# Kernel optimization log

Hardware: AMD Instinct MI355X
Metric: run time of the kernel (lower is better)

The kernel has to match this reference:

```python
import jax, jax.numpy as jnp
import numpy as np

D_MODEL = 1024
NUM_HEADS = 16
D_HEAD = D_MODEL // NUM_HEADS


def _rope(x):
    """Rotary embedding, lucidrains interleaved convention, applied along axis -2.

    x: (..., n, d). Positions are arange(n); freq_i = 10000**(-2i/d), each freq
    repeated twice (interleaved); rotate_half swaps adjacent pairs (-x2, x1).
    """
    n, d = x.shape[-2], x.shape[-1]
    inv_freq = 1.0 / (10000.0 ** (jnp.arange(0, d, 2, dtype=jnp.float32) / d))  # (d/2,)
    freqs = jnp.arange(n, dtype=jnp.float32)[:, None] * inv_freq[None, :]       # (n, d/2)
    emb = jnp.repeat(freqs, 2, axis=-1)                                         # (n, d)
    cos, sin = jnp.cos(emb).astype(x.dtype), jnp.sin(emb).astype(x.dtype)
    xp = x.reshape(x.shape[:-1] + (d // 2, 2))
    rot = jnp.stack([-xp[..., 1], xp[..., 0]], axis=-1).reshape(x.shape)
    return x * cos + rot * sin


def setup_inputs() -> dict:
    key = jax.random.key(0)
    ks = jax.random.split(key, 11)
    B, S = 4, 2048
    mk = lambda k, shape: (jax.random.normal(k, shape, dtype=jnp.float32) * 0.02)
    return {
        "query": jax.random.normal(ks[0], (B, S, D_MODEL), dtype=jnp.float32),
        "key": jax.random.normal(ks[1], (B, S, D_MODEL), dtype=jnp.float32),
        "value": jax.random.normal(ks[2], (B, S, D_MODEL), dtype=jnp.float32),
        "Wq": mk(ks[3], (D_MODEL, D_MODEL)), "bq": jnp.zeros((D_MODEL,), jnp.float32),
        "Wk": mk(ks[4], (D_MODEL, D_MODEL)), "bk": jnp.zeros((D_MODEL,), jnp.float32),
        "Wv": mk(ks[5], (D_MODEL, D_MODEL)), "bv": jnp.zeros((D_MODEL,), jnp.float32),
        "Wo": mk(ks[6], (D_MODEL, D_MODEL)), "bo": jnp.zeros((D_MODEL,), jnp.float32),
    }


def reference(query, key, value, Wq, bq, Wk, bk, Wv, bv, Wo, bo):
    B, S, _ = query.shape
    H, dh = NUM_HEADS, D_HEAD
    # projections (torch Linear: x @ W.T + b)
    q = (query @ Wq.T + bq).reshape(B, S, H, dh)           # (b, t, h, d)
    k = (key @ Wk.T + bk).reshape(B, S, H, dh).transpose(0, 2, 1, 3)   # (b, h, t, d)
    v = (value @ Wv.T + bv).reshape(B, S, H, dh).transpose(0, 2, 1, 3)  # (b, h, t, d)
    # Faithful to source: query rotated along axis -2 = HEADS axis (pre-permute),
    # key rotated along axis -2 = time axis.
    q = _rope(q)                                            # positions over heads (source quirk)
    k = _rope(k)                                            # positions over time
    q = q.transpose(0, 2, 1, 3)                             # (b, h, t, d)
    scores = jnp.einsum("bhqd,bhkd->bhqk", q, k) / jnp.sqrt(jnp.float32(D_MODEL))
    attn = jax.nn.softmax(scores, axis=-1)
    ctx = jnp.einsum("bhqk,bhkd->bhqd", attn, v)            # (b, h, t, d)
    ctx = ctx.transpose(0, 2, 1, 3).reshape(B, S, H * dh)   # (b, t, d_model)
    return ctx @ Wo.T + bo
```

## Files before the change

kernel.cpp:

```cpp
#include <hip/hip_runtime.h>

using u16 = unsigned short;
typedef __bf16 bf16x8 __attribute__((ext_vector_type(8)));
typedef __bf16 bf16x2 __attribute__((ext_vector_type(2)));
typedef float f32x4 __attribute__((ext_vector_type(4)));

#if __has_builtin(__builtin_amdgcn_exp2f)
#define QSCALE 0.04508422468443852f
#define FEXP(x) __builtin_amdgcn_exp2f(x)
#else
#define QSCALE 0.03125f
#define FEXP(x) __expf(x)
#endif

__device__ __forceinline__ u16 f2bf(float f) {
  unsigned u = __builtin_bit_cast(unsigned, f);
  u += 0x7FFFu + ((u >> 16) & 1u);
  return (u16)(u >> 16);
}

#define GLD_LDS16(g, l)                                                                   \
  __builtin_amdgcn_global_load_lds((const __attribute__((address_space(1))) void*)(g),    \
                                   (__attribute__((address_space(3))) void*)(l), 16, 0, 0)

__global__ void cvt_all(const float* __restrict__ q, const float* __restrict__ k,
                        const float* __restrict__ v, const float* __restrict__ wq,
                        const float* __restrict__ wk, const float* __restrict__ wv,
                        const float* __restrict__ wo, u16* __restrict__ oq,
                        u16* __restrict__ ok, u16* __restrict__ ov, u16* __restrict__ owq,
                        u16* __restrict__ owk, u16* __restrict__ owv, u16* __restrict__ owo) {
  const float* in;
  u16* out;
  int n4, base, nb;
  const int bidx = blockIdx.x;
  if (bidx < 1536) {
    const int which = bidx >> 9;
    in = which == 0 ? q : which == 1 ? k : v;
    out = which == 0 ? oq : which == 1 ? ok : ov;
    n4 = 2097152; base = bidx & 511; nb = 512;
  } else {
    const int which = (bidx - 1536) >> 6;
    in = which == 0 ? wq : which == 1 ? wk : which == 2 ? wv : wo;
    out = which == 0 ? owq : which == 1 ? owk : which == 2 ? owv : owo;
    n4 = 262144; base = (bidx - 1536) & 63; nb = 64;
  }
  int i = base * blockDim.x + threadIdx.x;
  const int st = nb * blockDim.x;
  for (; i < n4; i += st) {
    float4 x = reinterpret_cast<const float4*>(in)[i];
    ushort4 o = make_ushort4(f2bf(x.x), f2bf(x.y), f2bf(x.z), f2bf(x.w));
    reinterpret_cast<ushort4*>(out)[i] = o;
  }
}

template <int EPI>
__global__ __launch_bounds__(512, 4) void gemm_bt(const u16* __restrict__ A,
                                                  const u16* __restrict__ Bt,
                                                  const float* __restrict__ bias,
                                                  void* __restrict__ outp) {
  __shared__ u16 lA[2][128 * 64];
  __shared__ u16 lB[2][128 * 64];
  const int tid = threadIdx.x;
  const int l = tid & 63, w = tid >> 6;
  const int wr = w >> 2, wc = w & 3;
  const int l15 = l & 15, lg = l >> 4;
  const int bid = ((blockIdx.x & 7) << 6) | (blockIdx.x >> 3);
  const int br = bid >> 3, bc = bid & 7;

  f32x4 acc[4][2];
#pragma unroll
  for (int m = 0; m < 4; ++m)
#pragma unroll
    for (int n = 0; n < 2; ++n) acc[m][n] = f32x4{0.f, 0.f, 0.f, 0.f};

  const int srow = tid >> 3;
  const int gch = (tid & 7) ^ (srow & 7);
  const u16* Abase = A + (size_t)(br * 128 + srow) * 1024 + gch * 8;
  const u16* Bbase = Bt + (size_t)(bc * 128 + srow) * 1024 + gch * 8;

  auto stage = [&](int buf, int kk) {
    GLD_LDS16(Abase + kk, &lA[buf][tid * 8]);
    GLD_LDS16(Abase + (size_t)64 * 1024 + kk, &lA[buf][4096 + tid * 8]);
    GLD_LDS16(Bbase + kk, &lB[buf][tid * 8]);
    GLD_LDS16(Bbase + (size_t)64 * 1024 + kk, &lB[buf][4096 + tid * 8]);
  };

  auto compute = [&](int cur) {
#pragma unroll
    for (int ks = 0; ks < 2; ++ks) {
      const int c = (((ks * 4 + lg) ^ (l15 & 7)) << 3);
      bf16x8 af[4], bfr[2];
#pragma unroll
      for (int m = 0; m < 4; ++m)
        af[m] = *reinterpret_cast<const bf16x8*>(&lA[cur][(wr * 64 + m * 16 + l15) * 64 + c]);
#pragma unroll
      for (int n = 0; n < 2; ++n)
        bfr[n] = *reinterpret_cast<const bf16x8*>(&lB[cur][(wc * 32 + n * 16 + l15) * 64 + c]);
#pragma unroll
      for (int m = 0; m < 4; ++m)
#pragma unroll
        for (int n = 0; n < 2; ++n)
          acc[m][n] = __builtin_amdgcn_mfma_f32_16x16x32_bf16(af[m], bfr[n], acc[m][n], 0, 0, 0);
    }
  };

  stage(0, 0);
  asm volatile("s_waitcnt vmcnt(0)" ::: "memory");
  __builtin_amdgcn_s_barrier();
  __builtin_amdgcn_sched_barrier(0);

  for (int it = 0; it < 16; ++it) {
    const int cur = it & 1;
    if (it < 15) stage(cur ^ 1, (it + 1) * 64);
    compute(cur);
    if (it < 15) {
      asm volatile("s_waitcnt vmcnt(0)" ::: "memory");
      __builtin_amdgcn_s_barrier();
      __builtin_amdgcn_sched_barrier(0);
    }
  }

  const int row0 = br * 128 + wr * 64;
  const int col0 = bc * 128 + wc * 32;

  if constexpr (EPI == 0 || EPI == 1) {
    u16* out = reinterpret_cast<u16*>(outp);
#pragma unroll
    for (int n = 0; n < 2; ++n) {
      const int gn = col0 + n * 16 + l15;
      const float bv2 = bias[gn];
      const int p = (gn & 63) >> 1;
      const float invf = __expf((float)p * -0.28782313663f);
      float ss = 0.f, cc = 0.f;
      if constexpr (EPI == 0) {
        const float th = (float)(gn >> 6) * invf;
        sincosf(th, &ss, &cc);
      }
#pragma unroll
      for (int m = 0; m < 4; ++m) {
        const int gm0 = row0 + m * 16 + lg * 4;
#pragma unroll
        for (int r = 0; r < 4; ++r) {
          float x = acc[m][n][r] + bv2;
          if constexpr (EPI == 1) {
            const float th = (float)((gm0 + r) & 2047) * invf;
            sincosf(th, &ss, &cc);
          }
          const float xp = __shfl_xor(x, 1);
          float o = (gn & 1) ? fmaf(xp, ss, x * cc) : fmaf(-xp, ss, x * cc);
          if constexpr (EPI == 0) o *= QSCALE;
          out[(size_t)(gm0 + r) * 1024 + gn] = f2bf(o);
        }
      }
    }
  } else if constexpr (EPI == 2) {
    u16* vT = reinterpret_cast<u16*>(outp);
#pragma unroll
    for (int n = 0; n < 2; ++n) {
      const int gn = col0 + n * 16 + l15;
      const float bv2 = bias[gn];
      const int hh = gn >> 6, dd = gn & 63;
#pragma unroll
      for (int m = 0; m < 4; ++m) {
        const int gm0 = row0 + m * 16 + lg * 4;
        const int bb = gm0 >> 11, s0 = gm0 & 2047;
        ushort4 pk = make_ushort4(f2bf(acc[m][n][0] + bv2), f2bf(acc[m][n][1] + bv2),
                                  f2bf(acc[m][n][2] + bv2), f2bf(acc[m][n][3] + bv2));
        *reinterpret_cast<ushort4*>(vT + ((size_t)((bb * 16 + hh) * 64 + dd) * 2048 + s0)) = pk;
      }
    }
  } else {
    float* out = reinterpret_cast<float*>(outp);
#pragma unroll
    for (int n = 0; n < 2; ++n) {
      const int gn = col0 + n * 16 + l15;
      const float bv2 = bias[gn];
#pragma unroll
      for (int m = 0; m < 4; ++m) {
        const int gm0 = row0 + m * 16 + lg * 4;
#pragma unroll
        for (int r = 0; r < 4; ++r) out[(size_t)(gm0 + r) * 1024 + gn] = acc[m][n][r] + bv2;
      }
    }
  }
}

__global__ __launch_bounds__(512, 4) void attn_fwd(const u16* __restrict__ Q,
                                                   const u16* __restrict__ K,
                                                   const u16* __restrict__ Vt,
                                                   u16* __restrict__ ctx) {
  __shared__ u16 sK[3][64 * 64];
  __shared__ u16 sV[3][64 * 64];
  const int tid = threadIdx.x;
  const int l = tid & 63, w = tid >> 6;
  const int l15 = l & 15, lg = l >> 4;
  const int swz = (l15 & 7) << 3;
  const int wgid = ((blockIdx.x & 7) << 6) | (blockIdx.x >> 3);
  const int qt = wgid & 7, bh = wgid >> 3;
  const int b = bh >> 4, h = bh & 15;

  bf16x8 qf[2][2];
#pragma unroll
  for (int g = 0; g < 2; ++g) {
    const u16* qp =
        Q + (size_t)(b * 2048 + qt * 256 + w * 32 + g * 16 + l15) * 1024 + h * 64 + lg * 8;
    qf[g][0] = *reinterpret_cast<const bf16x8*>(qp);
    qf[g][1] = *reinterpret_cast<const bf16x8*>(qp + 32);
  }

  bf16x8 ones;
#pragma unroll
  for (int i = 0; i < 8; ++i) ones[i] = (__bf16)1.0f;

  f32x4 acc_l[2];
  f32x4 acc_o[2][4];
#pragma unroll
  for (int g = 0; g < 2; ++g) {
    acc_l[g] = f32x4{0.f, 0.f, 0.f, 0.f};
#pragma unroll
    for (int n = 0; n < 4; ++n) acc_o[g][n] = f32x4{0.f, 0.f, 0.f, 0.f};
  }

  const int srow = tid >> 3;
  const int scol = ((tid & 7) ^ (srow & 7)) * 8;
  const int krow = (srow & 0x23) | ((srow & 0x0C) << 1) | ((srow & 0x10) >> 2);
  const u16* Kbase = K + (size_t)(b * 2048 + krow) * 1024 + h * 64 + scol;
  const u16* Vbase = Vt + (size_t)(bh * 64 + srow) * 2048 + scol;

  auto stage = [&](int buf, int j) {
    GLD_LDS16(Kbase + (size_t)(j * 64) * 1024, &sK[buf][tid * 8]);
    GLD_LDS16(Vbase + j * 64, &sV[buf][tid * 8]);
  };

  stage(0, 0);
  stage(1, 1);
  asm volatile("s_waitcnt vmcnt(2)" ::: "memory");
  __builtin_amdgcn_s_barrier();
  __builtin_amdgcn_sched_barrier(0);

  int cur = 0, nx2 = 2;
  for (int j = 0; j < 32; ++j) {
    if (j < 30) stage(nx2, j + 2);

    const int c0 = (lg * 8) ^ swz;
    f32x4 accs0[4], accs1[4];
#pragma unroll
    for (int nk = 0; nk < 4; ++nk) {
      accs0[nk] = f32x4{0.f, 0.f, 0.f, 0.f};
      accs1[nk] = f32x4{0.f, 0.f, 0.f, 0.f};
    }

    __builtin_amdgcn_s_setprio(1);
#pragma unroll
    for (int nk = 0; nk < 4; ++nk) {
      bf16x8 kf0 = *reinterpret_cast<const bf16x8*>(&sK[cur][(nk * 16 + l15) * 64 + c0]);
      bf16x8 kf1 = *reinterpret_cast<const bf16x8*>(&sK[cur][(nk * 16 + l15) * 64 + (c0 ^ 32)]);
      accs0[nk] = __builtin_amdgcn_mfma_f32_16x16x32_bf16(kf0, qf[0][0], accs0[nk], 0, 0, 0);
      accs0[nk] = __builtin_amdgcn_mfma_f32_16x16x32_bf16(kf1, qf[0][1], accs0[nk], 0, 0, 0);
      accs1[nk] = __builtin_amdgcn_mfma_f32_16x16x32_bf16(kf0, qf[1][0], accs1[nk], 0, 0, 0);
      accs1[nk] = __builtin_amdgcn_mfma_f32_16x16x32_bf16(kf1, qf[1][1], accs1[nk], 0, 0, 0);
    }
    __builtin_amdgcn_s_setprio(0);

    unsigned wpk0[4][2], wpk1[4][2];
#pragma unroll
    for (int nk = 0; nk < 4; ++nk) {
      const float p0 = FEXP(accs0[nk][0]), p1 = FEXP(accs0[nk][1]);
      const float p2 = FEXP(accs0[nk][2]), p3 = FEXP(accs0[nk][3]);
      bf16x2 t0, t1;
      t0.x = (__bf16)p0; t0.y = (__bf16)p1;
      t1.x = (__bf16)p2; t1.y = (__bf16)p3;
      wpk0[nk][0] = __builtin_bit_cast(unsigned, t0);
      wpk0[nk][1] = __builtin_bit_cast(unsigned, t1);
    }

    __builtin_amdgcn_s_setprio(1);
#pragma unroll
    for (int ks = 0; ks < 2; ++ks) {
      const uint4 paw = make_uint4(wpk0[2 * ks][0], wpk0[2 * ks][1],
                                   wpk0[2 * ks + 1][0], wpk0[2 * ks + 1][1]);
      const bf16x8 pa = __builtin_bit_cast(bf16x8, paw);
      acc_l[0] = __builtin_amdgcn_mfma_f32_16x16x32_bf16(ones, pa, acc_l[0], 0, 0, 0);
#pragma unroll
      for (int n = 0; n < 4; ++n) {
        bf16x8 vf = *reinterpret_cast<const bf16x8*>(
            &sV[cur][(n * 16 + l15) * 64 + ((ks * 32 + lg * 8) ^ swz)]);
        acc_o[0][n] = __builtin_amdgcn_mfma_f32_16x16x32_bf16(vf, pa, acc_o[0][n], 0, 0, 0);
      }
    }
    __builtin_amdgcn_s_setprio(0);

#pragma unroll
    for (int nk = 0; nk < 4; ++nk) {
      const float p0 = FEXP(accs1[nk][0]), p1 = FEXP(accs1[nk][1]);
      const float p2 = FEXP(accs1[nk][2]), p3 = FEXP(accs1[nk][3]);
      bf16x2 t0, t1;
      t0.x = (__bf16)p0; t0.y = (__bf16)p1;
      t1.x = (__bf16)p2; t1.y = (__bf16)p3;
      wpk1[nk][0] = __builtin_bit_cast(unsigned, t0);
      wpk1[nk][1] = __builtin_bit_cast(unsigned, t1);
    }

    __builtin_amdgcn_s_setprio(1);
#pragma unroll
    for (int ks = 0; ks < 2; ++ks) {
      const uint4 paw = make_uint4(wpk1[2 * ks][0], wpk1[2 * ks][1],
                                   wpk1[2 * ks + 1][0], wpk1[2 * ks + 1][1]);
      const bf16x8 pa = __builtin_bit_cast(bf16x8, paw);
      acc_l[1] = __builtin_amdgcn_mfma_f32_16x16x32_bf16(ones, pa, acc_l[1], 0, 0, 0);
#pragma unroll
      for (int n = 0; n < 4; ++n) {
        bf16x8 vf = *reinterpret_cast<const bf16x8*>(
            &sV[cur][(n * 16 + l15) * 64 + ((ks * 32 + lg * 8) ^ swz)]);
        acc_o[1][n] = __builtin_amdgcn_mfma_f32_16x16x32_bf16(vf, pa, acc_o[1][n], 0, 0, 0);
      }
    }
    __builtin_amdgcn_s_setprio(0);

    if (j < 31) {
      if (j < 30)
        asm volatile("s_waitcnt vmcnt(2)" ::: "memory");
      else
        asm volatile("s_waitcnt vmcnt(0)" ::: "memory");
      __builtin_amdgcn_s_barrier();
      __builtin_amdgcn_sched_barrier(0);
    }
    cur = cur == 2 ? 0 : cur + 1;
    nx2 = nx2 == 2 ? 0 : nx2 + 1;
  }

#pragma unroll
  for (int g = 0; g < 2; ++g) {
    const float inv = 1.f / acc_l[g][0];
    u16* obase =
        ctx + (size_t)(b * 2048 + qt * 256 + w * 32 + g * 16 + l15) * 1024 + h * 64;
#pragma unroll
    for (int n = 0; n < 4; ++n) {
      ushort4 pk = make_ushort4(f2bf(acc_o[g][n][0] * inv), f2bf(acc_o[g][n][1] * inv),
                                f2bf(acc_o[g][n][2] * inv), f2bf(acc_o[g][n][3] * inv));
      *reinterpret_cast<ushort4*>(obase + n * 16 + lg * 4) = pk;
    }
  }
}

extern "C" void kernel_launch(void* const* d_in, const int* in_sizes, int n_in, void* d_out,
                              int out_size, void* d_ws, size_t ws_size, hipStream_t stream) {
  (void)in_sizes; (void)n_in; (void)out_size; (void)ws_size;
  const float* query = (const float*)d_in[0];
  const float* key = (const float*)d_in[1];
  const float* value = (const float*)d_in[2];
  const float* Wq = (const float*)d_in[3];
  const float* bq = (const float*)d_in[4];
  const float* Wk = (const float*)d_in[5];
  const float* bk = (const float*)d_in[6];
  const float* Wv = (const float*)d_in[7];
  const float* bv = (const float*)d_in[8];
  const float* Wo = (const float*)d_in[9];
  const float* bo = (const float*)d_in[10];

  char* ws = (char*)d_ws;
  const size_t MB = (size_t)1 << 20;
  u16* xq = (u16*)(ws + 0 * MB);
  u16* xk = (u16*)(ws + 16 * MB);
  u16* xv = (u16*)(ws + 32 * MB);
  u16* wqb = (u16*)(ws + 48 * MB);
  u16* wkb = (u16*)(ws + 50 * MB);
  u16* wvb = (u16*)(ws + 52 * MB);
  u16* wob = (u16*)(ws + 54 * MB);
  u16* qb = (u16*)(ws + 56 * MB);
  u16* kb = (u16*)(ws + 72 * MB);
  u16* vT = (u16*)(ws + 88 * MB);
  u16* cx = (u16*)(ws + 104 * MB);

  cvt_all<<<1792, 256, 0, stream>>>(query, key, value, Wq, Wk, Wv, Wo, xq, xk, xv, wqb, wkb,
                                    wvb, wob);

  gemm_bt<0><<<512, 512, 0, stream>>>(xq, wqb, bq, qb);
  gemm_bt<1><<<512, 512, 0, stream>>>(xk, wkb, bk, kb);
  gemm_bt<2><<<512, 512, 0, stream>>>(xv, wvb, bv, vT);
  attn_fwd<<<512, 512, 0, stream>>>(qb, kb, vT, cx);
  gemm_bt<3><<<512, 512, 0, stream>>>(cx, wob, bo, (float*)d_out);
}
```

Before: 195.3 us.

## Load GEMM B operand directly to registers and triple-buffer A in LDS

The projection GEMM no longer stages the B (weight) tile through shared memory. Each lane now reads its B fragments straight from global memory into registers. The A tile moves from double to triple buffering with a prefetch distance of two and partial vmcnt waits, which is meant to hide global latency and cut LDS traffic and footprint. In exchange, B reads are now direct uncoalesced 16-byte global loads that are duplicated across the wr wave rows and depend on cache hits. The vmcnt accounting also has to match the mixed direct and LDS loads exactly.

```diff
diff --git a/kernel.cpp b/kernel.cpp
--- a/kernel.cpp
+++ b/kernel.cpp
@@ -58,8 +58,7 @@
                                                   const u16* __restrict__ Bt,
                                                   const float* __restrict__ bias,
                                                   void* __restrict__ outp) {
-  __shared__ u16 lA[2][128 * 64];
-  __shared__ u16 lB[2][128 * 64];
+  __shared__ u16 lA[3][128 * 64];
   const int tid = threadIdx.x;
   const int l = tid & 63, w = tid >> 6;
   const int wr = w >> 2, wc = w & 3;
@@ -76,48 +75,55 @@
   const int srow = tid >> 3;
   const int gch = (tid & 7) ^ (srow & 7);
   const u16* Abase = A + (size_t)(br * 128 + srow) * 1024 + gch * 8;
-  const u16* Bbase = Bt + (size_t)(bc * 128 + srow) * 1024 + gch * 8;
-
-  auto stage = [&](int buf, int kk) {
+  const u16* Bp0 = Bt + (size_t)(bc * 128 + wc * 32 + l15) * 1024 + lg * 8;
+  const u16* Bp1 = Bp0 + (size_t)16 * 1024;
+
+  auto stageA = [&](int buf, int kk) {
     GLD_LDS16(Abase + kk, &lA[buf][tid * 8]);
     GLD_LDS16(Abase + (size_t)64 * 1024 + kk, &lA[buf][4096 + tid * 8]);
-    GLD_LDS16(Bbase + kk, &lB[buf][tid * 8]);
-    GLD_LDS16(Bbase + (size_t)64 * 1024 + kk, &lB[buf][4096 + tid * 8]);
   };
 
-  auto compute = [&](int cur) {
+  stageA(0, 0);
+  stageA(1, 64);
+  asm volatile("s_waitcnt vmcnt(2)" ::: "memory");
+  __builtin_amdgcn_s_barrier();
+  __builtin_amdgcn_sched_barrier(0);
+
+  int cur = 0, nx2 = 2;
+  for (int it = 0; it < 16; ++it) {
+    bf16x8 bfr[2][2];
+#pragma unroll
+    for (int ks = 0; ks < 2; ++ks) {
+      bfr[ks][0] = *reinterpret_cast<const bf16x8*>(Bp0 + it * 64 + ks * 32);
+      bfr[ks][1] = *reinterpret_cast<const bf16x8*>(Bp1 + it * 64 + ks * 32);
+    }
+    if (it < 14) stageA(nx2, (it + 2) * 64);
+
 #pragma unroll
     for (int ks = 0; ks < 2; ++ks) {
       const int c = (((ks * 4 + lg) ^ (l15 & 7)) << 3);
-      bf16x8 af[4], bfr[2];
+      bf16x8 af[4];
 #pragma unroll
       for (int m = 0; m < 4; ++m)
         af[m] = *reinterpret_cast<const bf16x8*>(&lA[cur][(wr * 64 + m * 16 + l15) * 64 + c]);
 #pragma unroll
-      for (int n = 0; n < 2; ++n)
-        bfr[n] = *reinterpret_cast<const bf16x8*>(&lB[cur][(wc * 32 + n * 16 + l15) * 64 + c]);
-#pragma unroll
       for (int m = 0; m < 4; ++m)
 #pragma unroll
         for (int n = 0; n < 2; ++n)
-          acc[m][n] = __builtin_amdgcn_mfma_f32_16x16x32_bf16(af[m], bfr[n], acc[m][n], 0, 0, 0);
-    }
-  };
-
-  stage(0, 0);
-  asm volatile("s_waitcnt vmcnt(0)" ::: "memory");
-  __builtin_amdgcn_s_barrier();
-  __builtin_amdgcn_sched_barrier(0);
-
-  for (int it = 0; it < 16; ++it) {
-    const int cur = it & 1;
-    if (it < 15) stage(cur ^ 1, (it + 1) * 64);
-    compute(cur);
+          acc[m][n] =
+              __builtin_amdgcn_mfma_f32_16x16x32_bf16(af[m], bfr[ks][n], acc[m][n], 0, 0, 0);
+    }
+
     if (it < 15) {
-      asm volatile("s_waitcnt vmcnt(0)" ::: "memory");
+      if (it < 14)
+        asm volatile("s_waitcnt vmcnt(2)" ::: "memory");
+      else
+        asm volatile("s_waitcnt vmcnt(0)" ::: "memory");
       __builtin_amdgcn_s_barrier();
       __builtin_amdgcn_sched_barrier(0);
     }
+    cur = cur == 2 ? 0 : cur + 1;
+    nx2 = nx2 == 2 ? 0 : nx2 + 1;
   }
 
   const int row0 = br * 128 + wr * 64;
```

Measured after the change: 256.3 us. 31.2% more time.
